# Kernel tuning notes

Hardware: AMD Instinct MI355X
Metric: run time of the kernel (lower is better)

## Reference

```python
import jax, jax.numpy as jnp
import numpy as np

EMBED, HEADS, LEVELS, POINTS = 256, 8, 4, 4
HD = EMBED // HEADS
BS, NQ = 2, 16384
SHAPES = [(128, 128), (64, 64), (32, 32), (16, 16)]  # (H, W) per level
NV = sum(h * w for h, w in SHAPES)
EPS = 1e-5


def layernorm(x, g, b):
    mu = jnp.mean(x, -1, keepdims=True)
    var = jnp.mean((x - mu) ** 2, -1, keepdims=True)
    return (x - mu) / jnp.sqrt(var + EPS) * g + b


def bilinear_sample(vl, loc, H, W):
    # vl: (bs, heads, H*W, hd); loc: (bs, nq, heads, P, 2) normalized [0,1]
    # grid_sample semantics: align_corners=False, zero padding
    x = loc[..., 0] * W - 0.5
    y = loc[..., 1] * H - 0.5
    x0 = jnp.floor(x)
    y0 = jnp.floor(y)
    lx, ly = x - x0, y - y0
    x0 = x0.astype(jnp.int32)
    y0 = y0.astype(jnp.int32)
    gather = jax.vmap(jax.vmap(lambda t, i: t[i]))  # over (bs, heads)
    acc = None
    for dx, dy, w in ((0, 0, (1 - lx) * (1 - ly)), (1, 0, lx * (1 - ly)),
                      (0, 1, (1 - lx) * ly), (1, 1, lx * ly)):
        xi, yi = x0 + dx, y0 + dy
        valid = ((xi >= 0) & (xi < W) & (yi >= 0) & (yi < H)).astype(vl.dtype)
        idx = jnp.clip(yi, 0, H - 1) * W + jnp.clip(xi, 0, W - 1)
        idx = idx.transpose(0, 2, 1, 3)           # (bs, heads, nq, P)
        g = gather(vl, idx)                       # (bs, heads, nq, P, hd)
        wv = (w * valid).transpose(0, 2, 1, 3)[..., None]
        acc = g * wv if acc is None else acc + g * wv
    return acc


def forward(lidar_feat, feat_flatten, ref_2d, spatial_shapes, level_start_index,
            q_pose, W_off, b_off, W_attn, b_attn, W_val, b_val, W_out, b_out,
            ln1_g, ln1_b, ffn_w1, ffn_w2, ln2_g, ln2_b):
    identity = lidar_feat                         # (nq, bs, C)
    q = (lidar_feat + q_pose).transpose(1, 0, 2)  # (bs, nq, C)
    bs, nq, C = q.shape
    v = feat_flatten.transpose(1, 0, 2) @ W_val + b_val
    v = v.reshape(bs, -1, HEADS, HD)
    off = (q @ W_off + b_off).reshape(bs, nq, HEADS, LEVELS, POINTS, 2)
    aw = (q @ W_attn + b_attn).reshape(bs, nq, HEADS, LEVELS * POINTS)
    aw = jax.nn.softmax(aw, -1).reshape(bs, nq, HEADS, LEVELS, POINTS)
    ss = np.asarray(spatial_shapes)               # static level shapes
    lsi = np.asarray(level_start_index)
    norm = jnp.asarray(ss[:, ::-1].copy(), q.dtype)  # (L, 2) [W, H]
    loc = ref_2d[:, :, None, :, None, :] + off / norm[None, None, None, :, None, :]
    out = jnp.zeros((bs, nq, HEADS, HD), q.dtype)
    for l in range(LEVELS):
        H, W = int(ss[l, 0]), int(ss[l, 1])
        s = int(lsi[l])
        vl = v[:, s:s + H * W].transpose(0, 2, 1, 3)   # (bs, heads, HW, hd)
        sampled = bilinear_sample(vl, loc[:, :, :, l], H, W)
        out = out + jnp.einsum('bhqpd,bqhp->bqhd', sampled, aw[:, :, :, l, :])
    out = out.reshape(bs, nq, C) @ W_out + b_out
    out = out.transpose(1, 0, 2) + identity       # residual (dropout=eval noop)
    x = layernorm(out, ln1_g, ln1_b)
    x = layernorm(jnp.maximum(x @ ffn_w1, 0.0) @ ffn_w2 + x, ln2_g, ln2_b)
    return x


def setup_inputs():
    key = jax.random.key(0)
    ks = jax.random.split(key, 16)
    starts = np.cumsum([0] + [h * w for h, w in SHAPES])[:-1]
    d = {
        'lidar_feat': jax.random.normal(ks[0], (NQ, BS, EMBED), jnp.float32),
        'feat_flatten': jax.random.normal(ks[1], (NV, BS, EMBED), jnp.float32),
        'ref_2d': jax.random.uniform(ks[2], (BS, NQ, LEVELS, 2), jnp.float32),
        'spatial_shapes': jnp.array(SHAPES, jnp.int32),
        'level_start_index': jnp.array(starts, jnp.int32),
        'q_pose': jax.random.normal(ks[3], (NQ, BS, EMBED), jnp.float32),
        'W_off': 0.02 * jax.random.normal(ks[4], (EMBED, HEADS * LEVELS * POINTS * 2), jnp.float32),
        'b_off': 2.0 * jax.random.normal(ks[5], (HEADS * LEVELS * POINTS * 2,), jnp.float32),
        'W_attn': 0.02 * jax.random.normal(ks[6], (EMBED, HEADS * LEVELS * POINTS), jnp.float32),
        'b_attn': jnp.zeros((HEADS * LEVELS * POINTS,), jnp.float32),
        'W_val': 0.02 * jax.random.normal(ks[7], (EMBED, EMBED), jnp.float32),
        'b_val': jnp.zeros((EMBED,), jnp.float32),
        'W_out': 0.02 * jax.random.normal(ks[8], (EMBED, EMBED), jnp.float32),
        'b_out': jnp.zeros((EMBED,), jnp.float32),
        'ln1_g': jnp.ones((EMBED,), jnp.float32),
        'ln1_b': jnp.zeros((EMBED,), jnp.float32),
        'ffn_w1': 0.02 * jax.random.normal(ks[9], (EMBED, EMBED), jnp.float32),
        'ffn_w2': 0.02 * jax.random.normal(ks[10], (EMBED, EMBED), jnp.float32),
        'ln2_g': jnp.ones((EMBED,), jnp.float32),
        'ln2_b': jnp.zeros((EMBED,), jnp.float32),
    }
    return d


def reference(lidar_feat, feat_flatten, ref_2d, spatial_shapes, level_start_index,
              q_pose, W_off, b_off, W_attn, b_attn, W_val, b_val, W_out, b_out,
              ln1_g, ln1_b, ffn_w1, ffn_w2, ln2_g, ln2_b):
    return forward(lidar_feat, feat_flatten, ref_2d, spatial_shapes,
                   level_start_index, q_pose, W_off, b_off, W_attn, b_attn,
                   W_val, b_val, W_out, b_out, ln1_g, ln1_b, ffn_w1, ffn_w2,
                   ln2_g, ln2_b)
```

## Files before the change

kernel.cpp:

```cpp
#include <hip/hip_runtime.h>
#include <cstdint>

#define EMBED 256
#define HEADS 8
#define LEVELS 4
#define POINTS 4
#define BS 2
#define NQ 16384
#define NV 21760
#define MQ (BS*NQ)
#define MV (BS*NV)
#define VAL_BLK 340
#define OA_BLK  256

typedef __attribute__((ext_vector_type(8))) short short8;
typedef __attribute__((ext_vector_type(4))) float f32x4;

__device__ __forceinline__ unsigned short f2bf(float f) {
    unsigned int u = __float_as_uint(f);
    u = (u + 0x7FFFu + ((u >> 16) & 1u)) >> 16;
    return (unsigned short)u;
}
__device__ __forceinline__ float bf2f(unsigned short h) {
    return __uint_as_float(((unsigned int)h) << 16);
}
__device__ __forceinline__ float bflo(unsigned int u) {
    return __uint_as_float(u << 16);
}
__device__ __forceinline__ float bfhi(unsigned int u) {
    return __uint_as_float(u & 0xFFFF0000u);
}
__device__ __forceinline__ void glds16(const unsigned short* g, unsigned short* l) {
    __builtin_amdgcn_global_load_lds((const __attribute__((address_space(1))) void*)g,
                                     (__attribute__((address_space(3))) void*)l, 16, 0, 0);
}

struct WtArgs {
    const float* src[6];
    unsigned short* dst[6];
    int n[6];
};
__global__ __launch_bounds__(256) void prep_wt(
    WtArgs a, const float* __restrict__ ref2d,
    int* __restrict__ bkt, int* __restrict__ hist)
{
    const int t = threadIdx.x, g = blockIdx.y, bx = blockIdx.x;
    if (g == 6) {
        if (bx < 64) {
#pragma unroll
            for (int i = 0; i < 2; ++i) {
                const int rb = bx * 512 + i * 256 + t;
                const float x = ref2d[(size_t)rb * 8 + 0];
                const float y = ref2d[(size_t)rb * 8 + 1];
                const int qx = min(15, max(0, (int)(x * 16.f)));
                const int qy = min(15, max(0, (int)(y * 16.f)));
                const int bv = (rb >> 14) * 256 + qy * 16 + qx;
                bkt[rb] = bv;
                atomicAdd(&hist[bv], 1);
            }
        }
        return;
    }
    const int N = a.n[g];
    const int e = bx * 256 + t;
    if (e >= 256 * N) return;
    const int k = e / N, n = e - k * N;
    a.dst[g][(size_t)n * 256 + k] = f2bf(a.src[g][e]);
}

template<int NCOLS>
__device__ __forceinline__ void gemm_core(
    unsigned short* As, unsigned short* Bs, int bx,
    const float* __restrict__ Af, const float* __restrict__ A2f, int inner,
    const unsigned short* __restrict__ Bt,
    const float* __restrict__ bias0, const float* __restrict__ bias1,
    unsigned short* __restrict__ lidarb, unsigned short* __restrict__ outh)
{
    constexpr int FN = NCOLS / 64;
    const int t = threadIdx.x, l = t & 63, w = t >> 6;
    const int wm = w >> 2, wn = w & 3;
    const int frow = l & 15, fgrp = l >> 4;
    const size_t brow = (size_t)bx * 128;

    const int fslot = fgrp ^ ((frow & 3) ^ ((frow >> 2) & 3));
    const int srow = l >> 2;
    const int sswz = (l & 3) ^ ((srow & 3) ^ ((srow >> 2) & 3));
    const unsigned short* gB0 = Bt + ((size_t)(w * 16 + srow)) * 256 + sswz * 8;

    const int arow_s = t >> 2, aslot_s = t & 3;
    const int grow = (int)brow + arow_s;
    const int bidx = grow / inner, nn = grow - bidx * inner;
    const size_t srcrow = (size_t)(nn * BS + bidx) * 256;
    const float* srcA = Af + srcrow;
    const float* srcA2 = A2f ? A2f + srcrow : nullptr;
    const int aswz_s = aslot_s ^ ((arow_s & 3) ^ ((arow_s >> 2) & 3));

    f32x4 acc[4][FN];
#pragma unroll
    for (int i = 0; i < 4; ++i)
#pragma unroll
        for (int j = 0; j < FN; ++j) acc[i][j] = f32x4{0.f, 0.f, 0.f, 0.f};

    float4 pA0 = *(const float4*)(srcA + aslot_s * 8);
    float4 pA1 = *(const float4*)(srcA + aslot_s * 8 + 4);
    float4 pC0, pC1;
    if (srcA2) { pC0 = *(const float4*)(srcA2 + aslot_s * 8);
                 pC1 = *(const float4*)(srcA2 + aslot_s * 8 + 4); }

    for (int k0 = 0; k0 < 256; k0 += 32) {
        glds16(gB0 + k0,         &Bs[w * 512]);
        glds16(gB0 + 32768 + k0, &Bs[(w + 8) * 512]);
        if constexpr (NCOLS == 384)
            glds16(gB0 + 65536 + k0, &Bs[(w + 16) * 512]);

        if (lidarb) {
            short8 lk;
            lk[0] = (short)f2bf(pA0.x); lk[1] = (short)f2bf(pA0.y);
            lk[2] = (short)f2bf(pA0.z); lk[3] = (short)f2bf(pA0.w);
            lk[4] = (short)f2bf(pA1.x); lk[5] = (short)f2bf(pA1.y);
            lk[6] = (short)f2bf(pA1.z); lk[7] = (short)f2bf(pA1.w);
            *reinterpret_cast<short8*>(lidarb + srcrow + k0 + aslot_s * 8) = lk;
        }

        float c[8] = {pA0.x, pA0.y, pA0.z, pA0.w, pA1.x, pA1.y, pA1.z, pA1.w};
        if (srcA2) {
            c[0] += pC0.x; c[1] += pC0.y; c[2] += pC0.z; c[3] += pC0.w;
            c[4] += pC1.x; c[5] += pC1.y; c[6] += pC1.z; c[7] += pC1.w;
        }
        short8 pk;
#pragma unroll
        for (int i = 0; i < 8; ++i) pk[i] = (short)f2bf(c[i]);
        *reinterpret_cast<short8*>(&As[arow_s * 32 + aswz_s * 8]) = pk;
        if (k0 + 32 < 256) {
            pA0 = *(const float4*)(srcA + k0 + 32 + aslot_s * 8);
            pA1 = *(const float4*)(srcA + k0 + 32 + aslot_s * 8 + 4);
            if (srcA2) { pC0 = *(const float4*)(srcA2 + k0 + 32 + aslot_s * 8);
                         pC1 = *(const float4*)(srcA2 + k0 + 32 + aslot_s * 8 + 4); }
        }
        __syncthreads();

        short8 af[4]; short8 bq[FN];
#pragma unroll
        for (int fm = 0; fm < 4; ++fm)
            af[fm] = *reinterpret_cast<const short8*>(&As[(wm * 64 + fm * 16 + frow) * 32 + fslot * 8]);
#pragma unroll
        for (int fn = 0; fn < FN; ++fn)
            bq[fn] = *reinterpret_cast<const short8*>(&Bs[(wn * (NCOLS / 4) + fn * 16 + frow) * 32 + fslot * 8]);
#pragma unroll
        for (int fm = 0; fm < 4; ++fm)
#pragma unroll
            for (int fn = 0; fn < FN; ++fn)
                acc[fm][fn] = __builtin_amdgcn_mfma_f32_16x16x32_bf16(af[fm], bq[fn], acc[fm][fn], 0, 0, 0);
        __syncthreads();
    }

#pragma unroll
    for (int fn = 0; fn < FN; ++fn) {
        const int col = wn * (NCOLS / 4) + fn * 16 + frow;
        float b = 0.f;
        if (NCOLS == 384) b = (col < 256) ? bias0[col] : bias1[col - 256];
        else              b = bias0[col];
#pragma unroll
        for (int fm = 0; fm < 4; ++fm)
#pragma unroll
            for (int j = 0; j < 4; ++j) {
                const size_t row = brow + wm * 64 + fm * 16 + fgrp * 4 + j;
                outh[row * NCOLS + col] = f2bf(acc[fm][fn][j] + b);
            }
    }
}

__global__ __launch_bounds__(512) void valoa_k(
    const float* __restrict__ feat, const float* __restrict__ lidar,
    const float* __restrict__ q_pose,
    const unsigned short* __restrict__ wt_val, const unsigned short* __restrict__ wt_oa,
    const float* __restrict__ b_val, const float* __restrict__ b_off,
    const float* __restrict__ b_attn,
    unsigned short* __restrict__ vb, unsigned short* __restrict__ oa,
    unsigned short* __restrict__ lidarb,
    const int* __restrict__ hist, const int* __restrict__ bkt,
    int* __restrict__ perm)
{
    __shared__ unsigned short As[128 * 32];
    __shared__ unsigned short Bs[384 * 32];
    const int bx = blockIdx.x;
    if (bx < VAL_BLK) {
        gemm_core<256>(As, Bs, bx, feat, nullptr, NV, wt_val, b_val, nullptr, nullptr, vb);
    } else if (bx < VAL_BLK + OA_BLK) {
        gemm_core<384>(As, Bs, bx - VAL_BLK, lidar, q_pose, NQ, wt_oa, b_off, b_attn, lidarb, oa);
    } else {
        int* s   = (int*)As;
        int* cur = ((int*)As) + 512;
        const int t = threadIdx.x;
        const int v = hist[t];
        s[t] = v;
        __syncthreads();
        int acc = v;
#pragma unroll
        for (int o = 1; o < 512; o <<= 1) {
            const int add = (t >= o) ? s[t - o] : 0;
            __syncthreads();
            acc += add;
            s[t] = acc;
            __syncthreads();
        }
        cur[t] = acc - v;
        __syncthreads();
#pragma unroll 4
        for (int i = 0; i < 64; ++i) {
            const int rb = i * 512 + t;
            const int pos = atomicAdd(&cur[bkt[rb]], 1);
            perm[pos] = rb;
        }
    }
}

__global__ __launch_bounds__(128) void sampler_k(
    const unsigned short* __restrict__ oa,
    const float* __restrict__ ref2d,
    const unsigned short* __restrict__ v,
    const int* __restrict__ perm,
    unsigned short* __restrict__ outh)
{
    const int bid = blockIdx.x;
    const int sbid = (bid & 7) * (MQ / 4 / 8) + (bid >> 3);
    const int q0 = sbid * 4;
    const int t = threadIdx.x;

    __shared__ uint2 s_d[4][8][4][17];

#pragma unroll
    for (int it = 0; it < 4; ++it) {
        const int item = t + it * 128;
        const int tq = item >> 7, hlp = item & 127;
        const int h = hlp >> 4, lp = hlp & 15, li = lp >> 2;
        const int rb = perm[q0 + tq];
        const int b = rb >> 14;

        const float2 refv = *(const float2*)(ref2d + (size_t)rb * 8 + li * 2);
        const ushort2 offu = *(const ushort2*)(oa + (size_t)rb * 384 + hlp * 2);
        const float ax = bf2f(oa[(size_t)rb * 384 + 256 + hlp]);

        float m = ax;
#pragma unroll
        for (int o = 1; o < 16; o <<= 1) m = fmaxf(m, __shfl_xor(m, o));
        const float e = __expf(ax - m);
        float sden = e;
#pragma unroll
        for (int o = 1; o < 16; o <<= 1) sden += __shfl_xor(sden, o);
        const float a = e / sden;

        const int Wl[4]  = {128, 64, 32, 16};
        const int S0l[4] = {0, 16384, 20480, 21504};
        const int Wi = Wl[li]; const float Wf = (float)Wi;
        const float x = (refv.x + bf2f(offu.x) / Wf) * Wf - 0.5f;
        const float y = (refv.y + bf2f(offu.y) / Wf) * Wf - 0.5f;
        const float x0f = floorf(x), y0f = floorf(y);
        const float lx = x - x0f, ly = y - y0f;
        const int x0 = (int)x0f, y0 = (int)y0f;
        const float cw[4] = {(1.f - lx) * (1.f - ly) * a, lx * (1.f - ly) * a,
                             (1.f - lx) * ly * a,          lx * ly * a};
        const int base = b * NV + S0l[li];
#pragma unroll
        for (int c = 0; c < 4; ++c) {
            const int xi = x0 + (c & 1), yi = y0 + (c >> 1);
            const bool val = (xi >= 0) & (xi < Wi) & (yi >= 0) & (yi < Wi);
            const int xc = min(max(xi, 0), Wi - 1), yc = min(max(yi, 0), Wi - 1);
            const unsigned int ofs = (unsigned int)(base + yc * Wi + xc) * 512u + h * 64u;
            s_d[tq][h][c][lp] = make_uint2(__float_as_uint(val ? cw[c] : 0.f), ofs);
        }
    }
    __syncthreads();

    const int tq = t >> 5, r = t & 31, h = r >> 2, dq = r & 3;
    const int rb = perm[q0 + tq], b = rb >> 14, qi = rb & (NQ - 1);
    const char* vq = (const char*)v + dq * 16u;
    float a0 = 0.f, a1 = 0.f, a2 = 0.f, a3 = 0.f;
    float a4 = 0.f, a5 = 0.f, a6 = 0.f, a7 = 0.f;
#pragma unroll
    for (int c = 0; c < 4; ++c) {
#pragma unroll
        for (int i = 0; i < 16; ++i) {
            const uint2 dd = s_d[tq][h][c][i];
            const uint4 raw = *(const uint4*)(vq + dd.y);
            const float wgt = __uint_as_float(dd.x);
            a0 += wgt * bflo(raw.x); a1 += wgt * bfhi(raw.x);
            a2 += wgt * bflo(raw.y); a3 += wgt * bfhi(raw.y);
            a4 += wgt * bflo(raw.z); a5 += wgt * bfhi(raw.z);
            a6 += wgt * bflo(raw.w); a7 += wgt * bfhi(raw.w);
        }
    }
    short8 o;
    o[0] = (short)f2bf(a0); o[1] = (short)f2bf(a1);
    o[2] = (short)f2bf(a2); o[3] = (short)f2bf(a3);
    o[4] = (short)f2bf(a4); o[5] = (short)f2bf(a5);
    o[6] = (short)f2bf(a6); o[7] = (short)f2bf(a7);
    *reinterpret_cast<short8*>(outh + (size_t)(qi * BS + b) * 256 + h * 32 + dq * 8) = o;
}

__global__ __launch_bounds__(512) void mega_k(
    const unsigned short* __restrict__ smp, const unsigned short* __restrict__ lidarb,
    const unsigned short* __restrict__ Wo, const unsigned short* __restrict__ W1,
    const unsigned short* __restrict__ W2, const float* __restrict__ b_out,
    const float* __restrict__ ln1g, const float* __restrict__ ln1b,
    const float* __restrict__ ln2g, const float* __restrict__ ln2b,
    float* __restrict__ outf)
{
    __shared__ unsigned short XH[64 * 256];
    __shared__ unsigned short Bs[256 * 32];
    __shared__ float2 sdLN[64][4];

    const int t = threadIdx.x, l = t & 63, w = t >> 6;
    const int wm = w >> 2, wn = w & 3;
    const int frow = l & 15, fgrp = l >> 4;
    const size_t brow = (size_t)blockIdx.x * 64;

    const int fslot = fgrp ^ ((frow & 3) ^ ((frow >> 2) & 3));
    const int srow = l >> 2;
    const int sswz = (l & 3) ^ ((srow & 3) ^ ((srow >> 2) & 3));

    const unsigned short* gA  = smp + (brow + (size_t)((w & 3) * 16 + srow)) * 256 + sswz * 8;
    const unsigned short* gWo = Wo + ((size_t)(w * 16 + srow)) * 256 + sswz * 8;
    const unsigned short* gW1 = W1 + ((size_t)(w * 16 + srow)) * 256 + sswz * 8;
    const unsigned short* gW2 = W2 + ((size_t)(w * 16 + srow)) * 256 + sswz * 8;

    f32x4 acc[2][4];
    f32x4 xres[2][4];

#pragma unroll
    for (int i = 0; i < 2; ++i)
#pragma unroll
        for (int j = 0; j < 4; ++j) acc[i][j] = f32x4{0.f, 0.f, 0.f, 0.f};

    for (int k0 = 0; k0 < 256; k0 += 32) {
        glds16(gWo + k0,         &Bs[w * 512]);
        glds16(gWo + 32768 + k0, &Bs[(w + 8) * 512]);
        if (w < 4) glds16(gA + k0, &XH[w * 512]);
        __syncthreads();
        short8 af[2], bq[4];
#pragma unroll
        for (int fm = 0; fm < 2; ++fm)
            af[fm] = *reinterpret_cast<const short8*>(&XH[(wm * 32 + fm * 16 + frow) * 32 + fslot * 8]);
#pragma unroll
        for (int fn = 0; fn < 4; ++fn)
            bq[fn] = *reinterpret_cast<const short8*>(&Bs[(wn * 64 + fn * 16 + frow) * 32 + fslot * 8]);
#pragma unroll
        for (int fm = 0; fm < 2; ++fm)
#pragma unroll
            for (int fn = 0; fn < 4; ++fn)
                acc[fm][fn] = __builtin_amdgcn_mfma_f32_16x16x32_bf16(af[fm], bq[fn], acc[fm][fn], 0, 0, 0);
        __syncthreads();
    }

#pragma unroll
    for (int fm = 0; fm < 2; ++fm)
#pragma unroll
        for (int fn = 0; fn < 4; ++fn) {
            const int col = wn * 64 + fn * 16 + frow;
            const float bv = b_out[col];
#pragma unroll
            for (int j = 0; j < 4; ++j) {
                const size_t row = brow + wm * 32 + fm * 16 + fgrp * 4 + j;
                acc[fm][fn][j] += bv + bf2f(lidarb[row * 256 + col]);
            }
        }
#pragma unroll
    for (int fm = 0; fm < 2; ++fm)
#pragma unroll
        for (int j = 0; j < 4; ++j) {
            float s1 = 0.f, s2 = 0.f;
#pragma unroll
            for (int fn = 0; fn < 4; ++fn) { const float x = acc[fm][fn][j]; s1 += x; s2 += x * x; }
#pragma unroll
            for (int o = 1; o < 16; o <<= 1) { s1 += __shfl_xor(s1, o); s2 += __shfl_xor(s2, o); }
            if (frow == 0) sdLN[wm * 32 + fm * 16 + fgrp * 4 + j][wn] = make_float2(s1, s2);
        }
    __syncthreads();
#pragma unroll
    for (int fm = 0; fm < 2; ++fm)
#pragma unroll
        for (int j = 0; j < 4; ++j) {
            const int rl = wm * 32 + fm * 16 + fgrp * 4 + j;
            const float2 p0 = sdLN[rl][0], p1 = sdLN[rl][1], p2 = sdLN[rl][2], p3 = sdLN[rl][3];
            const float s1 = p0.x + p1.x + p2.x + p3.x;
            const float s2 = p0.y + p1.y + p2.y + p3.y;
            const float mu = s1 * (1.f / 256.f);
            const float var = s2 * (1.f / 256.f) - mu * mu;
            const float rstd = rsqrtf(var + 1e-5f);
#pragma unroll
            for (int fn = 0; fn < 4; ++fn) {
                const int col = wn * 64 + fn * 16 + frow;
                const float y = (acc[fm][fn][j] - mu) * rstd * ln1g[col] + ln1b[col];
                xres[fm][fn][j] = y;
                const int ss = (col >> 3) ^ (rl & 7);
                XH[rl * 256 + ss * 8 + (col & 7)] = f2bf(y);
            }
        }
    __syncthreads();

#pragma unroll
    for (int i = 0; i < 2; ++i)
#pragma unroll
        for (int j = 0; j < 4; ++j) acc[i][j] = f32x4{0.f, 0.f, 0.f, 0.f};

    for (int k0 = 0; k0 < 256; k0 += 32) {
        glds16(gW1 + k0,         &Bs[w * 512]);
        glds16(gW1 + 32768 + k0, &Bs[(w + 8) * 512]);
        __syncthreads();
        short8 af[2], bq[4];
#pragma unroll
        for (int fm = 0; fm < 2; ++fm) {
            const int row = wm * 32 + fm * 16 + frow;
            const int ss = ((k0 >> 3) + fgrp) ^ (row & 7);
            af[fm] = *reinterpret_cast<const short8*>(&XH[row * 256 + ss * 8]);
        }
#pragma unroll
        for (int fn = 0; fn < 4; ++fn)
            bq[fn] = *reinterpret_cast<const short8*>(&Bs[(wn * 64 + fn * 16 + frow) * 32 + fslot * 8]);
#pragma unroll
        for (int fm = 0; fm < 2; ++fm)
#pragma unroll
            for (int fn = 0; fn < 4; ++fn)
                acc[fm][fn] = __builtin_amdgcn_mfma_f32_16x16x32_bf16(af[fm], bq[fn], acc[fm][fn], 0, 0, 0);
        __syncthreads();
    }

#pragma unroll
    for (int fm = 0; fm < 2; ++fm)
#pragma unroll
        for (int fn = 0; fn < 4; ++fn) {
            const int col = wn * 64 + fn * 16 + frow;
#pragma unroll
            for (int j = 0; j < 4; ++j) {
                const int rl = wm * 32 + fm * 16 + fgrp * 4 + j;
                const int ss = (col >> 3) ^ (rl & 7);
                XH[rl * 256 + ss * 8 + (col & 7)] = f2bf(fmaxf(acc[fm][fn][j], 0.f));
            }
        }
    __syncthreads();

#pragma unroll
    for (int i = 0; i < 2; ++i)
#pragma unroll
        for (int j = 0; j < 4; ++j) acc[i][j] = f32x4{0.f, 0.f, 0.f, 0.f};

    for (int k0 = 0; k0 < 256; k0 += 32) {
        glds16(gW2 + k0,         &Bs[w * 512]);
        glds16(gW2 + 32768 + k0, &Bs[(w + 8) * 512]);
        __syncthreads();
        short8 af[2], bq[4];
#pragma unroll
        for (int fm = 0; fm < 2; ++fm) {
            const int row = wm * 32 + fm * 16 + frow;
            const int ss = ((k0 >> 3) + fgrp) ^ (row & 7);
            af[fm] = *reinterpret_cast<const short8*>(&XH[row * 256 + ss * 8]);
        }
#pragma unroll
        for (int fn = 0; fn < 4; ++fn)
            bq[fn] = *reinterpret_cast<const short8*>(&Bs[(wn * 64 + fn * 16 + frow) * 32 + fslot * 8]);
#pragma unroll
        for (int fm = 0; fm < 2; ++fm)
#pragma unroll
            for (int fn = 0; fn < 4; ++fn)
                acc[fm][fn] = __builtin_amdgcn_mfma_f32_16x16x32_bf16(af[fm], bq[fn], acc[fm][fn], 0, 0, 0);
        __syncthreads();
    }

#pragma unroll
    for (int fm = 0; fm < 2; ++fm)
#pragma unroll
        for (int fn = 0; fn < 4; ++fn)
#pragma unroll
            for (int j = 0; j < 4; ++j) acc[fm][fn][j] += xres[fm][fn][j];
#pragma unroll
    for (int fm = 0; fm < 2; ++fm)
#pragma unroll
        for (int j = 0; j < 4; ++j) {
            float s1 = 0.f, s2 = 0.f;
#pragma unroll
            for (int fn = 0; fn < 4; ++fn) { const float x = acc[fm][fn][j]; s1 += x; s2 += x * x; }
#pragma unroll
            for (int o = 1; o < 16; o <<= 1) { s1 += __shfl_xor(s1, o); s2 += __shfl_xor(s2, o); }
            if (frow == 0) sdLN[wm * 32 + fm * 16 + fgrp * 4 + j][wn] = make_float2(s1, s2);
        }
    __syncthreads();
#pragma unroll
    for (int fm = 0; fm < 2; ++fm)
#pragma unroll
        for (int j = 0; j < 4; ++j) {
            const int rl = wm * 32 + fm * 16 + fgrp * 4 + j;
            const float2 p0 = sdLN[rl][0], p1 = sdLN[rl][1], p2 = sdLN[rl][2], p3 = sdLN[rl][3];
            const float s1 = p0.x + p1.x + p2.x + p3.x;
            const float s2 = p0.y + p1.y + p2.y + p3.y;
            const float mu = s1 * (1.f / 256.f);
            const float var = s2 * (1.f / 256.f) - mu * mu;
            const float rstd = rsqrtf(var + 1e-5f);
            const size_t row = brow + rl;
#pragma unroll
            for (int fn = 0; fn < 4; ++fn) {
                const int col = wn * 64 + fn * 16 + frow;
                outf[row * 256 + col] = (acc[fm][fn][j] - mu) * rstd * ln2g[col] + ln2b[col];
            }
        }
}

extern "C" void kernel_launch(void* const* d_in, const int* in_sizes, int n_in,
                              void* d_out, int out_size, void* d_ws, size_t ws_size,
                              hipStream_t stream)
{
    const float* lidar  = (const float*)d_in[0];
    const float* feat   = (const float*)d_in[1];
    const float* ref2d  = (const float*)d_in[2];
    const float* q_pose = (const float*)d_in[5];
    const float* W_off  = (const float*)d_in[6];
    const float* b_off  = (const float*)d_in[7];
    const float* W_attn = (const float*)d_in[8];
    const float* b_attn = (const float*)d_in[9];
    const float* W_val  = (const float*)d_in[10];
    const float* b_val  = (const float*)d_in[11];
    const float* W_out  = (const float*)d_in[12];
    const float* b_out  = (const float*)d_in[13];
    const float* ln1_g  = (const float*)d_in[14];
    const float* ln1_b  = (const float*)d_in[15];
    const float* ffn_w1 = (const float*)d_in[16];
    const float* ffn_w2 = (const float*)d_in[17];
    const float* ln2_g  = (const float*)d_in[18];
    const float* ln2_b  = (const float*)d_in[19];

    float* out = (float*)d_out;
    char*  ws  = (char*)d_ws;

    unsigned short* vb     = (unsigned short*)(ws + 0);
    unsigned short* oa     = (unsigned short*)(ws + 22282240);
    unsigned short* smp    = (unsigned short*)(ws + 47448064);
    unsigned short* lidarb = (unsigned short*)(ws + 64225280);
    unsigned short* wt     = (unsigned short*)(ws + 81002496);
    int* perm = (int*)(ws + 81723392);
    int* bkt  = (int*)(ws + 81854464);
    int* hist = (int*)(ws + 81985536);
    unsigned short* wt_val = wt;
    unsigned short* wt_oa  = wt + 65536;
    unsigned short* wt_out = wt + 163840;
    unsigned short* wt_f1  = wt + 229376;
    unsigned short* wt_f2  = wt + 294912;

    WtArgs wa;
    wa.src[0] = W_val;  wa.dst[0] = wt_val;          wa.n[0] = 256;
    wa.src[1] = W_off;  wa.dst[1] = wt_oa;           wa.n[1] = 256;
    wa.src[2] = W_attn; wa.dst[2] = wt_oa + 65536;   wa.n[2] = 128;
    wa.src[3] = W_out;  wa.dst[3] = wt_out;          wa.n[3] = 256;
    wa.src[4] = ffn_w1; wa.dst[4] = wt_f1;           wa.n[4] = 256;
    wa.src[5] = ffn_w2; wa.dst[5] = wt_f2;           wa.n[5] = 256;

    hipMemsetAsync(hist, 0, 2048, stream);

    prep_wt<<<dim3(384, 7), dim3(256), 0, stream>>>(wa, ref2d, bkt, hist);

    valoa_k<<<dim3(VAL_BLK + OA_BLK + 1), dim3(512), 0, stream>>>(
        feat, lidar, q_pose, wt_val, wt_oa, b_val, b_off, b_attn,
        vb, oa, lidarb, hist, bkt, perm);

    sampler_k<<<dim3(MQ / 4), dim3(128), 0, stream>>>(oa, ref2d, vb, perm, smp);

    mega_k<<<dim3(MQ / 64), dim3(512), 0, stream>>>(
        smp, lidarb, wt_out, wt_f1, wt_f2, b_out,
        ln1_g, ln1_b, ln2_g, ln2_b, out);
}
```

Baseline: 216.6 us.

## Give each sampler query its own wavefront and drop the block barrier

```diff
diff --git a/kernel.cpp b/kernel.cpp
--- a/kernel.cpp
+++ b/kernel.cpp
@@ -23,12 +23,6 @@
 }
 __device__ __forceinline__ float bf2f(unsigned short h) {
     return __uint_as_float(((unsigned int)h) << 16);
-}
-__device__ __forceinline__ float bflo(unsigned int u) {
-    return __uint_as_float(u << 16);
-}
-__device__ __forceinline__ float bfhi(unsigned int u) {
-    return __uint_as_float(u & 0xFFFF0000u);
 }
 __device__ __forceinline__ void glds16(const unsigned short* g, unsigned short* l) {
     __builtin_amdgcn_global_load_lds((const __attribute__((address_space(1))) void*)g,
@@ -215,7 +209,7 @@
     }
 }
 
-__global__ __launch_bounds__(128) void sampler_k(
+__global__ __launch_bounds__(256, 8) void sampler_k(
     const unsigned short* __restrict__ oa,
     const float* __restrict__ ref2d,
     const unsigned short* __restrict__ v,
@@ -226,16 +220,18 @@
     const int sbid = (bid & 7) * (MQ / 4 / 8) + (bid >> 3);
     const int q0 = sbid * 4;
     const int t = threadIdx.x;
+    const int tq = t >> 6;
+    const int l = t & 63;
 
     __shared__ uint2 s_d[4][8][4][17];
 
-#pragma unroll
-    for (int it = 0; it < 4; ++it) {
-        const int item = t + it * 128;
-        const int tq = item >> 7, hlp = item & 127;
+    const int rb = perm[q0 + tq];
+    const int b = rb >> 14, qi = rb & (NQ - 1);
+
+#pragma unroll
+    for (int it = 0; it < 2; ++it) {
+        const int hlp = it * 64 + l;
         const int h = hlp >> 4, lp = hlp & 15, li = lp >> 2;
-        const int rb = perm[q0 + tq];
-        const int b = rb >> 14;
 
         const float2 refv = *(const float2*)(ref2d + (size_t)rb * 8 + li * 2);
         const ushort2 offu = *(const ushort2*)(oa + (size_t)rb * 384 + hlp * 2);
@@ -270,32 +266,29 @@
             s_d[tq][h][c][lp] = make_uint2(__float_as_uint(val ? cw[c] : 0.f), ofs);
         }
     }
-    __syncthreads();
-
-    const int tq = t >> 5, r = t & 31, h = r >> 2, dq = r & 3;
-    const int rb = perm[q0 + tq], b = rb >> 14, qi = rb & (NQ - 1);
-    const char* vq = (const char*)v + dq * 16u;
+
+    asm volatile("s_waitcnt lgkmcnt(0)" ::: "memory");
+    __builtin_amdgcn_sched_barrier(0);
+
+    const int h = l >> 3, dq = l & 7;
+    const char* vq = (const char*)v + dq * 8u;
+    const uint2* dp = &s_d[tq][h][0][0];
     float a0 = 0.f, a1 = 0.f, a2 = 0.f, a3 = 0.f;
-    float a4 = 0.f, a5 = 0.f, a6 = 0.f, a7 = 0.f;
 #pragma unroll
     for (int c = 0; c < 4; ++c) {
 #pragma unroll
         for (int i = 0; i < 16; ++i) {
-            const uint2 dd = s_d[tq][h][c][i];
-            const uint4 raw = *(const uint4*)(vq + dd.y);
+            const uint2 dd = dp[c * 17 + i];
+            const uint2 raw = *(const uint2*)(vq + dd.y);
             const float wgt = __uint_as_float(dd.x);
-            a0 += wgt * bflo(raw.x); a1 += wgt * bfhi(raw.x);
-            a2 += wgt * bflo(raw.y); a3 += wgt * bfhi(raw.y);
-            a4 += wgt * bflo(raw.z); a5 += wgt * bfhi(raw.z);
-            a6 += wgt * bflo(raw.w); a7 += wgt * bfhi(raw.w);
-        }
-    }
-    short8 o;
-    o[0] = (short)f2bf(a0); o[1] = (short)f2bf(a1);
-    o[2] = (short)f2bf(a2); o[3] = (short)f2bf(a3);
-    o[4] = (short)f2bf(a4); o[5] = (short)f2bf(a5);
-    o[6] = (short)f2bf(a6); o[7] = (short)f2bf(a7);
-    *reinterpret_cast<short8*>(outh + (size_t)(qi * BS + b) * 256 + h * 32 + dq * 8) = o;
+            a0 += wgt * __uint_as_float(raw.x << 16);
+            a1 += wgt * __uint_as_float(raw.x & 0xFFFF0000u);
+            a2 += wgt * __uint_as_float(raw.y << 16);
+            a3 += wgt * __uint_as_float(raw.y & 0xFFFF0000u);
+        }
+    }
+    ushort4 o; o.x = f2bf(a0); o.y = f2bf(a1); o.z = f2bf(a2); o.w = f2bf(a3);
+    *(ushort4*)(outh + (size_t)(qi * BS + b) * 256 + h * 32 + dq * 4) = o;
 }
 
 __global__ __launch_bounds__(512) void mega_k(
@@ -560,7 +553,7 @@
         feat, lidar, q_pose, wt_val, wt_oa, b_val, b_off, b_attn,
         vb, oa, lidarb, hist, bkt, perm);
 
-    sampler_k<<<dim3(MQ / 4), dim3(128), 0, stream>>>(oa, ref2d, vb, perm, smp);
+    sampler_k<<<dim3(MQ / 4), dim3(256), 0, stream>>>(oa, ref2d, vb, perm, smp);
 
     mega_k<<<dim3(MQ / 64), dim3(512), 0, stream>>>(
         smp, lidarb, wt_out, wt_f1, wt_f2, b_out,
```

New measurement: 229.8 us. 1.06x slower.
